# Kernel tuning notes

Measured on AMD Instinct MI355X. Metric: run time of the kernel, lower is better.

Reference implementation:

```python
import jax, jax.numpy as jnp
import numpy as np

N = 100000   # nodes
E = 600000   # edges
D = 128      # d_model
R = 200      # num_relations


def setup_inputs() -> dict:
    key = jax.random.key(0)
    ks = jax.random.split(key, 12)
    def nrm(k, shape, scale=0.02):
        return jax.random.normal(k, shape, jnp.float32) * scale
    return dict(
        node_features=jax.random.normal(ks[0], (N, D), jnp.float32),
        edge_index=jax.random.randint(ks[1], (2, E), 0, N),
        edge_type=jax.random.randint(ks[2], (E,), 0, R),
        rel_embed=nrm(ks[3], (R, D)),
        msg_w1=nrm(ks[4], (2 * D, D)), msg_b1=jnp.zeros((D,), jnp.float32),
        msg_w2=nrm(ks[5], (D, D)), msg_b2=jnp.zeros((D,), jnp.float32),
        attn_w1=nrm(ks[6], (2 * D, D)), attn_b1=jnp.zeros((D,), jnp.float32),
        attn_w2=nrm(ks[7], (D, 1)), attn_b2=jnp.zeros((1,), jnp.float32),
        ln1_g=jnp.ones((D,), jnp.float32), ln1_b=jnp.zeros((D,), jnp.float32),
        ffn_w1=nrm(ks[8], (D, 4 * D)), ffn_b1=jnp.zeros((4 * D,), jnp.float32),
        ffn_w2=nrm(ks[9], (4 * D, D)), ffn_b2=jnp.zeros((D,), jnp.float32),
        ln2_g=jnp.ones((D,), jnp.float32), ln2_b=jnp.zeros((D,), jnp.float32),
    )


def layer_norm(x, g, b, eps=1e-5):
    mu = x.mean(-1, keepdims=True)
    var = ((x - mu) ** 2).mean(-1, keepdims=True)
    return (x - mu) * jax.lax.rsqrt(var + eps) * g + b


def reference(node_features, edge_index, edge_type, rel_embed,
              msg_w1, msg_b1, msg_w2, msg_b2,
              attn_w1, attn_b1, attn_w2, attn_b2,
              ln1_g, ln1_b, ffn_w1, ffn_b1, ffn_w2, ffn_b2,
              ln2_g, ln2_b):
    Nn = node_features.shape[0]
    src, dst = edge_index[0], edge_index[1]
    # gather + edge message MLP
    src_feat = node_features[src]              # [E, D]
    rel_feat = rel_embed[edge_type]            # [E, D]
    h = jnp.concatenate([src_feat, rel_feat], axis=-1)          # [E, 2D]
    messages = jax.nn.relu(h @ msg_w1 + msg_b1) @ msg_w2 + msg_b2  # [E, D]
    # edge attention logits
    a_in = jnp.concatenate([node_features[dst], messages], axis=-1)  # [E, 2D]
    attn_raw = (jax.nn.leaky_relu(a_in @ attn_w1 + attn_b1, 0.2) @ attn_w2 + attn_b2)[:, 0]  # [E]
    # two-pass segment softmax over destination nodes
    attn_max = jax.ops.segment_max(attn_raw, dst, num_segments=Nn)   # [N]
    attn_exp = jnp.exp(attn_raw - attn_max[dst])                      # [E]
    attn_sum = jax.ops.segment_sum(attn_exp, dst, num_segments=Nn)   # [N]
    attn_w = attn_exp / (attn_sum[dst] + 1e-8)                        # [E]
    # scatter-add weighted messages
    aggr = jax.ops.segment_sum(attn_w[:, None] * messages, dst, num_segments=Nn)  # [N, D]
    x = layer_norm(node_features + aggr, ln1_g, ln1_b)
    ffn = jax.nn.gelu(x @ ffn_w1 + ffn_b1, approximate=False) @ ffn_w2 + ffn_b2
    return layer_norm(x + ffn, ln2_g, ln2_b)
```

## Files before the change

kernel.cpp:

```cpp
#include <hip/hip_runtime.h>
#include <hip/hip_bf16.h>

#define NN 100000
#define NE 600000
#define DD 128
#define RR 200
#define SCAN_NB ((NN + 255) / 256)

typedef __attribute__((ext_vector_type(8))) short bf16x8;
typedef __attribute__((ext_vector_type(4))) float f32x4;

__device__ __forceinline__ unsigned int bfbits(float x) {
    return (unsigned int)__builtin_bit_cast(unsigned short, __float2bfloat16(x));
}
__device__ __forceinline__ unsigned int pk2(float a, float b) {
    return bfbits(a) | (bfbits(b) << 16);
}
__device__ __forceinline__ unsigned short bf16s(float x) {
    return __builtin_bit_cast(unsigned short, __float2bfloat16(x));
}
__device__ __forceinline__ float unbf(unsigned short u) {
    return __builtin_bit_cast(float, ((unsigned int)u) << 16);
}
__device__ __forceinline__ float unlo(unsigned int u) {
    return __builtin_bit_cast(float, u << 16);
}
__device__ __forceinline__ float unhi(unsigned int u) {
    return __builtin_bit_cast(float, u & 0xffff0000u);
}

__device__ __forceinline__ void gload_lds16(const void* g, void* l) {
    __builtin_amdgcn_global_load_lds(
        (const __attribute__((address_space(1))) void*)g,
        (__attribute__((address_space(3))) void*)l, 16, 0, 0);
}

__global__ void k_initc(int* __restrict__ cnt) {
    int i = blockIdx.x * 256 + threadIdx.x;
    if (i < NN) cnt[i] = 0;
}

__global__ void k_hist(const int* __restrict__ dst, int* __restrict__ cnt) {
    int e = blockIdx.x * 256 + threadIdx.x;
    if (e < NE) atomicAdd(&cnt[dst[e]], 1);
}

__global__ void k_scanA(const int* __restrict__ cnt, int* __restrict__ bsum) {
    __shared__ int red[256];
    int i = blockIdx.x * 256 + threadIdx.x;
    red[threadIdx.x] = (i < NN) ? cnt[i] : 0;
    __syncthreads();
    for (int off = 128; off >= 1; off >>= 1) {
        if (threadIdx.x < off) red[threadIdx.x] += red[threadIdx.x + off];
        __syncthreads();
    }
    if (threadIdx.x == 0) bsum[blockIdx.x] = red[0];
}

__global__ void k_scanB(int* __restrict__ bsum) {
    __shared__ int sh[512];
    int t = threadIdx.x;
    int v = (t < SCAN_NB) ? bsum[t] : 0;
    sh[t] = v;
    __syncthreads();
    for (int off = 1; off < 512; off <<= 1) {
        int add = (t >= off) ? sh[t - off] : 0;
        __syncthreads();
        sh[t] += add;
        __syncthreads();
    }
    if (t < SCAN_NB) bsum[t] = sh[t] - v;
}

__global__ void k_scanC(const int* __restrict__ cnt, const int* __restrict__ bsum,
                        int* __restrict__ row_start, int* __restrict__ cursor) {
    __shared__ int sh[256];
    int i = blockIdx.x * 256 + threadIdx.x;
    int t = threadIdx.x;
    int v = (i < NN) ? cnt[i] : 0;
    sh[t] = v;
    __syncthreads();
    for (int off = 1; off < 256; off <<= 1) {
        int add = (t >= off) ? sh[t - off] : 0;
        __syncthreads();
        sh[t] += add;
        __syncthreads();
    }
    if (i < NN) {
        int ex = bsum[blockIdx.x] + sh[t] - v;
        row_start[i] = ex;
        cursor[i] = ex;
    }
}

__global__ void k_bucket(const int* __restrict__ src, const int* __restrict__ dst,
                         const int* __restrict__ etype, int* __restrict__ cursor,
                         int* __restrict__ srcs, int* __restrict__ ets,
                         int* __restrict__ dsts) {
    int e = blockIdx.x * 256 + threadIdx.x;
    if (e < NE) {
        int d = dst[e];
        int p = atomicAdd(&cursor[d], 1);
        srcs[p] = src[e];
        ets[p]  = etype[e];
        dsts[p] = d;
    }
}

__global__ void k_setup(const float* __restrict__ mw1, const float* __restrict__ mb1,
                        const float* __restrict__ mw2, const float* __restrict__ mb2,
                        const float* __restrict__ aw1, const float* __restrict__ rel,
                        const float* __restrict__ fw1, const float* __restrict__ fw2,
                        unsigned short* __restrict__ mw1p,
                        unsigned short* __restrict__ mw2p,
                        unsigned short* __restrict__ awTp,
                        unsigned short* __restrict__ mwBp,
                        unsigned short* __restrict__ fw1p,
                        unsigned short* __restrict__ fw2p,
                        unsigned short* __restrict__ relcb,
                        float* __restrict__ zb) {
    int idx = blockIdx.x * 256 + threadIdx.x;
    if (idx < 16384) {
        int i = idx & 7, l = (idx >> 3) & 63, ks = (idx >> 9) & 3, nt = idx >> 11;
        int k = ks * 32 + (l >> 4) * 8 + i, n = nt * 16 + (l & 15);
        mw1p[idx] = bf16s(mw1[k * 128 + n]);
    } else if (idx < 32768) {
        int j = idx - 16384;
        int i = j & 7, l = (j >> 3) & 63, ks = (j >> 9) & 3, nt = j >> 11;
        int k = ks * 32 + (l >> 4) * 8 + i, n = nt * 16 + (l & 15);
        mw2p[j] = bf16s(mw2[k * 128 + n]);
    } else if (idx < 49152) {
        int j = idx - 32768;
        int i = j & 7, l = (j >> 3) & 63, ks = (j >> 9) & 3, nt = j >> 11;
        int k = ks * 32 + (l >> 4) * 8 + i, n = nt * 16 + (l & 15);
        awTp[j] = bf16s(aw1[k * 128 + n]);
    } else if (idx < 65536) {
        int j = idx - 49152;
        int i = j & 7, l = (j >> 3) & 63, ks = (j >> 9) & 3, nt = j >> 11;
        int k = ks * 32 + (l >> 4) * 8 + i, n = nt * 16 + (l & 15);
        float s = 0.0f;
        for (int j2 = 0; j2 < 128; ++j2)
            s = fmaf(mw2[k * 128 + j2], aw1[(128 + j2) * 128 + n], s);
        mwBp[j] = bf16s(s);
    } else if (idx < 131072) {
        int j = idx - 65536;
        int i = j & 7, l = (j >> 3) & 63, ks = (j >> 9) & 3, nt = j >> 11;
        int k = ks * 32 + (l >> 4) * 8 + i, n = nt * 16 + (l & 15);
        fw1p[j] = bf16s(fw1[k * 512 + n]);
    } else if (idx < 196608) {
        int j = idx - 131072;
        int i = j & 7, l = (j >> 3) & 63, ks = (j >> 9) & 15, nt = j >> 13;
        int k = ks * 32 + (l >> 4) * 8 + i, n = nt * 16 + (l & 15);
        fw2p[j] = bf16s(fw2[k * 128 + n]);
    } else if (idx < 222208) {
        int j = idx - 196608;
        int r = j >> 7, n = j & 127;
        float s = mb1[n];
        for (int k = 0; k < 128; ++k)
            s = fmaf(rel[r * 128 + k], mw1[(128 + k) * 128 + n], s);
        relcb[j] = bf16s(s);
    } else if (idx < 222336) {
        int n = idx - 222208;
        float s = 0.0f;
        for (int j2 = 0; j2 < 128; ++j2)
            s = fmaf(mb2[j2], aw1[(128 + j2) * 128 + n], s);
        zb[n] = s;
    }
}

__global__ __launch_bounds__(256) void k_prepnfa(
    const float* __restrict__ nf, const unsigned short* __restrict__ awTp,
    const float* __restrict__ ab1,
    unsigned short* __restrict__ nfb, unsigned short* __restrict__ nfa)
{
    __shared__ alignas(16) unsigned short XB[64 * 128];
    const int t = threadIdx.x;
    const int w = t >> 6, l = t & 63;
    const int wm = w >> 1, wn = w & 1;
    const int lm = l & 15, lk = l >> 4;
    const int n0 = blockIdx.x * 64;

    {
        const int row = t >> 2, seg = t & 3;
        long ng = n0 + row; if (ng >= NN) ng = NN - 1;
        const float* sp = nf + ng * DD + seg * 32;
        uint4 o[4];
        #pragma unroll
        for (int i = 0; i < 4; ++i) {
            float4 f0 = *reinterpret_cast<const float4*>(sp + i * 8);
            float4 f1 = *reinterpret_cast<const float4*>(sp + i * 8 + 4);
            o[i].x = pk2(f0.x, f0.y); o[i].y = pk2(f0.z, f0.w);
            o[i].z = pk2(f1.x, f1.y); o[i].w = pk2(f1.z, f1.w);
        }
        if (n0 + row < NN) {
            #pragma unroll
            for (int i = 0; i < 4; ++i)
                *reinterpret_cast<uint4*>(&nfb[(size_t)(n0 + row) * DD + (seg * 4 + i) * 8]) = o[i];
        }
        #pragma unroll
        for (int i = 0; i < 4; ++i) {
            int c = seg * 4 + i, slot = c ^ (row & 7);
            *reinterpret_cast<uint4*>(&XB[row * 128 + slot * 8]) = o[i];
        }
    }
    __syncthreads();

    f32x4 acc[2][4];
    #pragma unroll
    for (int mf = 0; mf < 2; ++mf)
        #pragma unroll
        for (int nfr = 0; nfr < 4; ++nfr) acc[mf][nfr] = (f32x4){0.f, 0.f, 0.f, 0.f};

    #pragma unroll
    for (int ks = 0; ks < 4; ++ks) {
        bf16x8 a[2];
        #pragma unroll
        for (int mf = 0; mf < 2; ++mf) {
            int m = wm * 32 + mf * 16 + lm;
            int slot = (ks * 4 + lk) ^ (m & 7);
            a[mf] = *reinterpret_cast<const bf16x8*>(&XB[m * 128 + slot * 8]);
        }
        #pragma unroll
        for (int nfr = 0; nfr < 4; ++nfr) {
            int nt = wn * 4 + nfr;
            bf16x8 b = *reinterpret_cast<const bf16x8*>(&awTp[((nt * 4 + ks) * 64 + l) * 8]);
            acc[0][nfr] = __builtin_amdgcn_mfma_f32_16x16x32_bf16(a[0], b, acc[0][nfr], 0, 0, 0);
            acc[1][nfr] = __builtin_amdgcn_mfma_f32_16x16x32_bf16(a[1], b, acc[1][nfr], 0, 0, 0);
        }
    }
    __syncthreads();

    #pragma unroll
    for (int nfr = 0; nfr < 4; ++nfr) {
        int n = wn * 64 + nfr * 16 + lm;
        float bv = ab1[n];
        #pragma unroll
        for (int mf = 0; mf < 2; ++mf)
            #pragma unroll
            for (int r = 0; r < 4; ++r) {
                int m = wm * 32 + mf * 16 + lk * 4 + r;
                XB[m * 128 + n] = bf16s(acc[mf][nfr][r] + bv);
            }
    }
    __syncthreads();

    #pragma unroll
    for (int j = 0; j < 4; ++j) {
        int q = j * 256 + t;
        int row = q >> 4, c16 = q & 15;
        if (n0 + row < NN)
            *reinterpret_cast<uint4*>(&nfa[(size_t)(n0 + row) * DD + c16 * 8]) =
                *reinterpret_cast<const uint4*>(&XB[row * 128 + c16 * 8]);
    }
}

__global__ __launch_bounds__(512) void k_edge(
    const unsigned short* __restrict__ nfb, const int* __restrict__ srcs,
    const int* __restrict__ dsts, const int* __restrict__ ets,
    const unsigned short* __restrict__ nfa, const unsigned short* __restrict__ relcb,
    const unsigned short* __restrict__ mw1p, const unsigned short* __restrict__ mwBp,
    const float* __restrict__ zb, const float* __restrict__ aw2,
    const float* __restrict__ ab2,
    unsigned short* __restrict__ hid_out, float* __restrict__ attn_raw)
{
    __shared__ alignas(16) unsigned short S[64 * 128];
    __shared__ alignas(16) unsigned short H[64 * 128];
    __shared__ float RED[64][4];

    const int t = threadIdx.x;
    const int w = t >> 6, l = t & 63;
    const int wm = w >> 2, wn = w & 3;
    const int lm = l & 15, lk = l >> 4;
    const int lrow = l >> 4, lslot = l & 15;
    const int e0 = blockIdx.x * 64;

    #pragma unroll
    for (int it = 0; it < 2; ++it) {
        int rb = w * 8 + it * 4;
        int row = rb + lrow;
        int c = lslot ^ (row & 7);
        gload_lds16(nfb + (size_t)srcs[e0 + row] * DD + c * 8, &S[rb * 128]);
    }
    #pragma unroll
    for (int it = 0; it < 2; ++it) {
        int rb = w * 8 + it * 4;
        int row = rb + lrow;
        int c = lslot ^ (row & 7);
        gload_lds16(relcb + (size_t)ets[e0 + row] * DD + c * 8, &H[rb * 128]);
    }
    __syncthreads();

    {
        f32x4 acc1[2][2];
        #pragma unroll
        for (int mf = 0; mf < 2; ++mf)
            #pragma unroll
            for (int nfr = 0; nfr < 2; ++nfr) acc1[mf][nfr] = (f32x4){0.f, 0.f, 0.f, 0.f};

        #pragma unroll
        for (int ks = 0; ks < 4; ++ks) {
            bf16x8 a[2];
            #pragma unroll
            for (int mf = 0; mf < 2; ++mf) {
                int m = wm * 32 + mf * 16 + lm;
                int slot = (ks * 4 + lk) ^ (m & 7);
                a[mf] = *reinterpret_cast<const bf16x8*>(&S[m * 128 + slot * 8]);
            }
            #pragma unroll
            for (int nfr = 0; nfr < 2; ++nfr) {
                int nt = wn * 2 + nfr;
                bf16x8 b = *reinterpret_cast<const bf16x8*>(&mw1p[((nt * 4 + ks) * 64 + l) * 8]);
                acc1[0][nfr] = __builtin_amdgcn_mfma_f32_16x16x32_bf16(a[0], b, acc1[0][nfr], 0, 0, 0);
                acc1[1][nfr] = __builtin_amdgcn_mfma_f32_16x16x32_bf16(a[1], b, acc1[1][nfr], 0, 0, 0);
            }
        }
        #pragma unroll
        for (int nfr = 0; nfr < 2; ++nfr) {
            int n = (wn * 2 + nfr) * 16 + lm;
            #pragma unroll
            for (int mf = 0; mf < 2; ++mf)
                #pragma unroll
                for (int r = 0; r < 4; ++r) {
                    int m = wm * 32 + mf * 16 + lk * 4 + r;
                    int sl = m * 128 + ((n >> 3) ^ (m & 7)) * 8 + (n & 7);
                    float v = acc1[mf][nfr][r] + unbf(H[sl]);
                    v = fmaxf(v, 0.0f);
                    H[sl] = bf16s(v);
                }
        }
    }
    __syncthreads();

    #pragma unroll
    for (int j = 0; j < 2; ++j) {
        int q = j * 512 + t;
        int row = q >> 4, c16 = q & 15;
        int slot = c16 ^ (row & 7);
        *reinterpret_cast<uint4*>(&hid_out[(size_t)(e0 + row) * DD + c16 * 8]) =
            *reinterpret_cast<const uint4*>(&H[row * 128 + slot * 8]);
    }
    #pragma unroll
    for (int it = 0; it < 2; ++it) {
        int rb = w * 8 + it * 4;
        int row = rb + lrow;
        int c = lslot ^ (row & 7);
        gload_lds16(nfa + (size_t)dsts[e0 + row] * DD + c * 8, &S[rb * 128]);
    }

    f32x4 acc[2][2];
    #pragma unroll
    for (int mf = 0; mf < 2; ++mf)
        #pragma unroll
        for (int nfr = 0; nfr < 2; ++nfr) acc[mf][nfr] = (f32x4){0.f, 0.f, 0.f, 0.f};

    #pragma unroll
    for (int ks = 0; ks < 4; ++ks) {
        bf16x8 a[2];
        #pragma unroll
        for (int mf = 0; mf < 2; ++mf) {
            int m = wm * 32 + mf * 16 + lm;
            int slot = (ks * 4 + lk) ^ (m & 7);
            a[mf] = *reinterpret_cast<const bf16x8*>(&H[m * 128 + slot * 8]);
        }
        #pragma unroll
        for (int nfr = 0; nfr < 2; ++nfr) {
            int nt = wn * 2 + nfr;
            bf16x8 b = *reinterpret_cast<const bf16x8*>(&mwBp[((nt * 4 + ks) * 64 + l) * 8]);
            acc[0][nfr] = __builtin_amdgcn_mfma_f32_16x16x32_bf16(a[0], b, acc[0][nfr], 0, 0, 0);
            acc[1][nfr] = __builtin_amdgcn_mfma_f32_16x16x32_bf16(a[1], b, acc[1][nfr], 0, 0, 0);
        }
    }
    __syncthreads();

    {
        float zbv[2], aw2v[2];
        #pragma unroll
        for (int nfr = 0; nfr < 2; ++nfr) {
            int nc = (wn * 2 + nfr) * 16 + lm;
            zbv[nfr] = zb[nc];
            aw2v[nfr] = aw2[nc];
        }
        #pragma unroll
        for (int mf = 0; mf < 2; ++mf)
            #pragma unroll
            for (int r = 0; r < 4; ++r) {
                int m = wm * 32 + mf * 16 + lk * 4 + r;
                float s = 0.0f;
                #pragma unroll
                for (int nfr = 0; nfr < 2; ++nfr) {
                    int nc = (wn * 2 + nfr) * 16 + lm;
                    float v = acc[mf][nfr][r] + zbv[nfr]
                            + unbf(S[m * 128 + ((nc >> 3) ^ (m & 7)) * 8 + (nc & 7)]);
                    v = (v > 0.0f) ? v : 0.2f * v;
                    s = fmaf(v, aw2v[nfr], s);
                }
                s += __shfl_xor(s, 1, 64);
                s += __shfl_xor(s, 2, 64);
                s += __shfl_xor(s, 4, 64);
                s += __shfl_xor(s, 8, 64);
                if (lm == 0) RED[m][wn] = s;
            }
    }
    __syncthreads();

    if (t < 64) {
        attn_raw[e0 + t] = RED[t][0] + RED[t][1] + RED[t][2] + RED[t][3] + ab2[0];
    }
}

__global__ __launch_bounds__(256) void k_aggr(
    const unsigned short* __restrict__ hid, const float* __restrict__ raw,
    const int* __restrict__ row_start, const int* __restrict__ cnt,
    unsigned short* __restrict__ haggrb)
{
    const int l = threadIdx.x & 63;
    const int n = blockIdx.x * 4 + (threadIdx.x >> 6);
    if (n >= NN) return;
    const int rs = row_start[n], deg = cnt[n];

    float m = -INFINITY;
    for (int j = l; j < deg; j += 64) m = fmaxf(m, raw[rs + j]);
    #pragma unroll
    for (int off = 32; off >= 1; off >>= 1) m = fmaxf(m, __shfl_xor(m, off, 64));

    float s = 0.0f;
    for (int j = l; j < deg; j += 64) s += expf(raw[rs + j] - m);
    #pragma unroll
    for (int off = 32; off >= 1; off >>= 1) s += __shfl_xor(s, off, 64);
    const float rinv = 1.0f / (s + 1e-8f);

    float a0 = 0.0f, a1 = 0.0f;
    for (int j = 0; j < deg; ++j) {
        float w = expf(raw[rs + j] - m) * rinv;
        unsigned int v = *reinterpret_cast<const unsigned int*>(
            &hid[(size_t)(rs + j) * DD + l * 2]);
        a0 = fmaf(w, unlo(v), a0);
        a1 = fmaf(w, unhi(v), a1);
    }
    *reinterpret_cast<unsigned int*>(&haggrb[(size_t)n * DD + l * 2]) = pk2(a0, a1);
}

__global__ __launch_bounds__(512) void k_node(
    const float* __restrict__ nf, const unsigned short* __restrict__ haggrb,
    const unsigned short* __restrict__ mw2p, const float* __restrict__ mb2,
    const float* __restrict__ g1, const float* __restrict__ b1,
    const unsigned short* __restrict__ fw1p, const float* __restrict__ fb1,
    const unsigned short* __restrict__ fw2p, const float* __restrict__ fb2,
    const float* __restrict__ g2, const float* __restrict__ b2,
    float* __restrict__ out)
{
    __shared__ alignas(16) unsigned short XB[64 * 128];
    __shared__ alignas(16) unsigned short HB[64 * 256];

    const int t = threadIdx.x;
    const int w = t >> 6, l = t & 63;
    const int wm = w >> 2, wn = w & 3;
    const int lm = l & 15, lk = l >> 4;
    const int lrow = l >> 4, lslot = l & 15;
    const int row = t >> 3;
    const int q = t & 7;
    const long n0 = (long)blockIdx.x * 64;
    const long rg = n0 + row;
    const long rc = (rg < NN) ? rg : (NN - 1);

    unsigned short* HG = HB;
    #pragma unroll
    for (int it = 0; it < 2; ++it) {
        int rb = w * 8 + it * 4;
        int rr = rb + lrow;
        long grow = n0 + rr; if (grow >= NN) grow = NN - 1;
        int c = lslot ^ (rr & 7);
        gload_lds16(haggrb + grow * DD + c * 8, &HG[rb * 128]);
    }
    __syncthreads();

    {
        f32x4 acc0[2][2];
        #pragma unroll
        for (int mf = 0; mf < 2; ++mf)
            #pragma unroll
            for (int nfr = 0; nfr < 2; ++nfr) acc0[mf][nfr] = (f32x4){0.f, 0.f, 0.f, 0.f};

        #pragma unroll
        for (int ks = 0; ks < 4; ++ks) {
            bf16x8 a[2];
            #pragma unroll
            for (int mf = 0; mf < 2; ++mf) {
                int m = wm * 32 + mf * 16 + lm;
                int slot = (ks * 4 + lk) ^ (m & 7);
                a[mf] = *reinterpret_cast<const bf16x8*>(&HG[m * 128 + slot * 8]);
            }
            #pragma unroll
            for (int nfr = 0; nfr < 2; ++nfr) {
                int nt = wn * 2 + nfr;
                bf16x8 b = *reinterpret_cast<const bf16x8*>(&mw2p[((nt * 4 + ks) * 64 + l) * 8]);
                acc0[0][nfr] = __builtin_amdgcn_mfma_f32_16x16x32_bf16(a[0], b, acc0[0][nfr], 0, 0, 0);
                acc0[1][nfr] = __builtin_amdgcn_mfma_f32_16x16x32_bf16(a[1], b, acc0[1][nfr], 0, 0, 0);
            }
        }
        #pragma unroll
        for (int nfr = 0; nfr < 2; ++nfr) {
            int n = (wn * 2 + nfr) * 16 + lm;
            float bv = mb2[n];
            #pragma unroll
            for (int mf = 0; mf < 2; ++mf)
                #pragma unroll
                for (int r = 0; r < 4; ++r) {
                    int m = wm * 32 + mf * 16 + lk * 4 + r;
                    XB[m * 128 + ((n >> 3) ^ (m & 7)) * 8 + (n & 7)] = bf16s(acc0[mf][nfr][r] + bv);
                }
        }
    }
    __syncthreads();

    float xr[16];
    float s = 0.0f, ss = 0.0f;
    {
        const float* xp = nf + rc * DD + q * 16;
        #pragma unroll
        for (int i = 0; i < 2; ++i) {
            int c = q * 2 + i, slot = c ^ (row & 7);
            uint4 v = *reinterpret_cast<const uint4*>(&XB[row * 128 + slot * 8]);
            float f[8];
            f[0] = unlo(v.x); f[1] = unhi(v.x); f[2] = unlo(v.y); f[3] = unhi(v.y);
            f[4] = unlo(v.z); f[5] = unhi(v.z); f[6] = unlo(v.w); f[7] = unhi(v.w);
            float4 a = *reinterpret_cast<const float4*>(xp + i * 8);
            float4 b = *reinterpret_cast<const float4*>(xp + i * 8 + 4);
            float vv[8] = {a.x + f[0], a.y + f[1], a.z + f[2], a.w + f[3],
                           b.x + f[4], b.y + f[5], b.z + f[6], b.w + f[7]};
            #pragma unroll
            for (int j = 0; j < 8; ++j) {
                xr[i * 8 + j] = vv[j];
                s += vv[j];
                ss = fmaf(vv[j], vv[j], ss);
            }
        }
    }
    s  += __shfl_xor(s, 1, 64);  s  += __shfl_xor(s, 2, 64);  s  += __shfl_xor(s, 4, 64);
    ss += __shfl_xor(ss, 1, 64); ss += __shfl_xor(ss, 2, 64); ss += __shfl_xor(ss, 4, 64);
    {
        float mu = s * (1.0f / DD);
        float var = ss * (1.0f / DD) - mu * mu;
        float rstd = rsqrtf(var + 1e-5f);
        #pragma unroll
        for (int i = 0; i < 4; ++i) {
            float4 gv = *reinterpret_cast<const float4*>(g1 + q * 16 + i * 4);
            float4 bv = *reinterpret_cast<const float4*>(b1 + q * 16 + i * 4);
            xr[i * 4 + 0] = (xr[i * 4 + 0] - mu) * rstd * gv.x + bv.x;
            xr[i * 4 + 1] = (xr[i * 4 + 1] - mu) * rstd * gv.y + bv.y;
            xr[i * 4 + 2] = (xr[i * 4 + 2] - mu) * rstd * gv.z + bv.z;
            xr[i * 4 + 3] = (xr[i * 4 + 3] - mu) * rstd * gv.w + bv.w;
        }
        #pragma unroll
        for (int i = 0; i < 2; ++i) {
            int c = q * 2 + i, slot = c ^ (row & 7);
            uint4 v;
            v.x = pk2(xr[i * 8 + 0], xr[i * 8 + 1]);
            v.y = pk2(xr[i * 8 + 2], xr[i * 8 + 3]);
            v.z = pk2(xr[i * 8 + 4], xr[i * 8 + 5]);
            v.w = pk2(xr[i * 8 + 6], xr[i * 8 + 7]);
            *reinterpret_cast<uint4*>(&XB[row * 128 + slot * 8]) = v;
        }
    }
    __syncthreads();

    f32x4 acc2[2][2];
    #pragma unroll
    for (int mf = 0; mf < 2; ++mf)
        #pragma unroll
        for (int nfr = 0; nfr < 2; ++nfr) acc2[mf][nfr] = (f32x4){0.f, 0.f, 0.f, 0.f};

    #pragma unroll
    for (int half = 0; half < 2; ++half) {
        f32x4 acc[2][4];
        #pragma unroll
        for (int mf = 0; mf < 2; ++mf)
            #pragma unroll
            for (int nfr = 0; nfr < 4; ++nfr) acc[mf][nfr] = (f32x4){0.f, 0.f, 0.f, 0.f};

        #pragma unroll
        for (int ks = 0; ks < 4; ++ks) {
            bf16x8 a[2];
            #pragma unroll
            for (int mf = 0; mf < 2; ++mf) {
                int m = wm * 32 + mf * 16 + lm;
                int slot = (ks * 4 + lk) ^ (m & 7);
                a[mf] = *reinterpret_cast<const bf16x8*>(&XB[m * 128 + slot * 8]);
            }
            #pragma unroll
            for (int nfr = 0; nfr < 4; ++nfr) {
                int nt = half * 16 + wn * 4 + nfr;
                bf16x8 b = *reinterpret_cast<const bf16x8*>(&fw1p[((nt * 4 + ks) * 64 + l) * 8]);
                acc[0][nfr] = __builtin_amdgcn_mfma_f32_16x16x32_bf16(a[0], b, acc[0][nfr], 0, 0, 0);
                acc[1][nfr] = __builtin_amdgcn_mfma_f32_16x16x32_bf16(a[1], b, acc[1][nfr], 0, 0, 0);
            }
        }
        #pragma unroll
        for (int nfr = 0; nfr < 4; ++nfr) {
            int nl = (wn * 4 + nfr) * 16 + lm;
            float bv = fb1[half * 256 + nl];
            #pragma unroll
            for (int mf = 0; mf < 2; ++mf)
                #pragma unroll
                for (int r = 0; r < 4; ++r) {
                    int m = wm * 32 + mf * 16 + lk * 4 + r;
                    float h = acc[mf][nfr][r] + bv;
                    float e = __expf(h * -1.702f);
                    float gvv = h * __builtin_amdgcn_rcpf(1.0f + e);
                    HB[m * 256 + (((nl >> 3) ^ (m & 7)) * 8) + (nl & 7)] = bf16s(gvv);
                }
        }
        __syncthreads();

        #pragma unroll
        for (int ks = 0; ks < 8; ++ks) {
            bf16x8 a[2];
            #pragma unroll
            for (int mf = 0; mf < 2; ++mf) {
                int m = wm * 32 + mf * 16 + lm;
                int slot = (ks * 4 + lk) ^ (m & 7);
                a[mf] = *reinterpret_cast<const bf16x8*>(&HB[m * 256 + slot * 8]);
            }
            #pragma unroll
            for (int nfr = 0; nfr < 2; ++nfr) {
                int nt = wn * 2 + nfr;
                int kg = half * 8 + ks;
                bf16x8 b = *reinterpret_cast<const bf16x8*>(&fw2p[((nt * 16 + kg) * 64 + l) * 8]);
                acc2[0][nfr] = __builtin_amdgcn_mfma_f32_16x16x32_bf16(a[0], b, acc2[0][nfr], 0, 0, 0);
                acc2[1][nfr] = __builtin_amdgcn_mfma_f32_16x16x32_bf16(a[1], b, acc2[1][nfr], 0, 0, 0);
            }
        }
        __syncthreads();
    }

    #pragma unroll
    for (int nfr = 0; nfr < 2; ++nfr) {
        int n = (wn * 2 + nfr) * 16 + lm;
        float bv = fb2[n];
        #pragma unroll
        for (int mf = 0; mf < 2; ++mf)
            #pragma unroll
            for (int r = 0; r < 4; ++r) {
                int m = wm * 32 + mf * 16 + lk * 4 + r;
                XB[m * 128 + (((n >> 3) ^ (m & 7)) * 8) + (n & 7)] = bf16s(acc2[mf][nfr][r] + bv);
            }
    }
    __syncthreads();

    float s2 = 0.0f, ss2 = 0.0f;
    #pragma unroll
    for (int i = 0; i < 2; ++i) {
        int c = q * 2 + i, slot = c ^ (row & 7);
        uint4 v = *reinterpret_cast<const uint4*>(&XB[row * 128 + slot * 8]);
        float f[8];
        f[0] = unlo(v.x); f[1] = unhi(v.x); f[2] = unlo(v.y); f[3] = unhi(v.y);
        f[4] = unlo(v.z); f[5] = unhi(v.z); f[6] = unlo(v.w); f[7] = unhi(v.w);
        #pragma unroll
        for (int j = 0; j < 8; ++j) {
            float vv = xr[i * 8 + j] + f[j];
            xr[i * 8 + j] = vv;
            s2 += vv;
            ss2 = fmaf(vv, vv, ss2);
        }
    }
    s2  += __shfl_xor(s2, 1, 64);  s2  += __shfl_xor(s2, 2, 64);  s2  += __shfl_xor(s2, 4, 64);
    ss2 += __shfl_xor(ss2, 1, 64); ss2 += __shfl_xor(ss2, 2, 64); ss2 += __shfl_xor(ss2, 4, 64);
    {
        float mu = s2 * (1.0f / DD);
        float var = ss2 * (1.0f / DD) - mu * mu;
        float rstd = rsqrtf(var + 1e-5f);
        if (rg < NN) {
            float* op = out + rg * DD + q * 16;
            #pragma unroll
            for (int i = 0; i < 4; ++i) {
                float4 gv = *reinterpret_cast<const float4*>(g2 + q * 16 + i * 4);
                float4 bv = *reinterpret_cast<const float4*>(b2 + q * 16 + i * 4);
                float4 o;
                o.x = (xr[i * 4 + 0] - mu) * rstd * gv.x + bv.x;
                o.y = (xr[i * 4 + 1] - mu) * rstd * gv.y + bv.y;
                o.z = (xr[i * 4 + 2] - mu) * rstd * gv.z + bv.z;
                o.w = (xr[i * 4 + 3] - mu) * rstd * gv.w + bv.w;
                *reinterpret_cast<float4*>(op + i * 4) = o;
            }
        }
    }
}

extern "C" void kernel_launch(void* const* d_in, const int* in_sizes, int n_in,
                              void* d_out, int out_size, void* d_ws, size_t ws_size,
                              hipStream_t stream)
{
    const float* nf  = (const float*)d_in[0];
    const int*   ei  = (const int*)d_in[1];
    const int*   et  = (const int*)d_in[2];
    const float* rel = (const float*)d_in[3];
    const float* mw1 = (const float*)d_in[4];
    const float* mb1 = (const float*)d_in[5];
    const float* mw2 = (const float*)d_in[6];
    const float* mb2 = (const float*)d_in[7];
    const float* aw1 = (const float*)d_in[8];
    const float* ab1 = (const float*)d_in[9];
    const float* aw2 = (const float*)d_in[10];
    const float* ab2 = (const float*)d_in[11];
    const float* g1  = (const float*)d_in[12];
    const float* b1  = (const float*)d_in[13];
    const float* fw1 = (const float*)d_in[14];
    const float* fb1 = (const float*)d_in[15];
    const float* fw2 = (const float*)d_in[16];
    const float* fb2 = (const float*)d_in[17];
    const float* g2  = (const float*)d_in[18];
    const float* b2  = (const float*)d_in[19];
    float* out = (float*)d_out;

    char* ws = (char*)d_ws;
    size_t off = 0;
    auto alloc = [&](size_t bytes) -> char* {
        char* p = ws + off;
        off += (bytes + 255) & ~(size_t)255;
        return p;
    };
    unsigned short* hid = (unsigned short*)alloc((size_t)NE * DD * 2);
    float* attn_raw = (float*)alloc((size_t)NE * 4);
    unsigned short* haggrb = (unsigned short*)alloc((size_t)NN * DD * 2);
    unsigned short* nfa = (unsigned short*)alloc((size_t)NN * DD * 2);
    unsigned short* nfb = (unsigned short*)alloc((size_t)NN * DD * 2);
    unsigned short* relcb = (unsigned short*)alloc((size_t)RR * DD * 2);
    float* zb  = (float*)alloc((size_t)128 * 4);
    int* cnt       = (int*)alloc((size_t)NN * 4);
    int* row_start = (int*)alloc((size_t)NN * 4);
    int* cursor    = (int*)alloc((size_t)NN * 4);
    int* srcs      = (int*)alloc((size_t)NE * 4);
    int* ets       = (int*)alloc((size_t)NE * 4);
    int* dsts      = (int*)alloc((size_t)NE * 4);
    int* bsum      = (int*)alloc((size_t)SCAN_NB * 4);
    unsigned short* mw1p = (unsigned short*)alloc(16384 * 2);
    unsigned short* mw2p = (unsigned short*)alloc(16384 * 2);
    unsigned short* awTp = (unsigned short*)alloc(16384 * 2);
    unsigned short* mwBp = (unsigned short*)alloc(16384 * 2);
    unsigned short* fw1p = (unsigned short*)alloc(65536 * 2);
    unsigned short* fw2p = (unsigned short*)alloc(65536 * 2);

    const int* srcp = ei;
    const int* dstp = ei + NE;

    hipLaunchKernelGGL(k_initc, dim3(SCAN_NB), dim3(256), 0, stream, cnt);
    hipLaunchKernelGGL(k_hist, dim3((NE + 255) / 256), dim3(256), 0, stream, dstp, cnt);
    hipLaunchKernelGGL(k_scanA, dim3(SCAN_NB), dim3(256), 0, stream, cnt, bsum);
    hipLaunchKernelGGL(k_scanB, dim3(1), dim3(512), 0, stream, bsum);
    hipLaunchKernelGGL(k_scanC, dim3(SCAN_NB), dim3(256), 0, stream, cnt, bsum, row_start, cursor);
    hipLaunchKernelGGL(k_bucket, dim3((NE + 255) / 256), dim3(256), 0, stream,
                       srcp, dstp, et, cursor, srcs, ets, dsts);
    hipLaunchKernelGGL(k_setup, dim3(869), dim3(256), 0, stream,
                       mw1, mb1, mw2, mb2, aw1, rel, fw1, fw2,
                       mw1p, mw2p, awTp, mwBp, fw1p, fw2p, relcb, zb);
    hipLaunchKernelGGL(k_prepnfa, dim3((NN + 63) / 64), dim3(256), 0, stream,
                       nf, awTp, ab1, nfb, nfa);
    hipLaunchKernelGGL(k_edge, dim3(NE / 64), dim3(512), 0, stream,
                       nfb, srcs, dsts, ets, nfa, relcb,
                       mw1p, mwBp, zb, aw2, ab2,
                       hid, attn_raw);
    hipLaunchKernelGGL(k_aggr, dim3((NN + 3) / 4), dim3(256), 0, stream,
                       hid, attn_raw, row_start, cnt, haggrb);
    hipLaunchKernelGGL(k_node, dim3((NN + 63) / 64), dim3(512), 0, stream,
                       nf, haggrb, mw2p, mb2, g1, b1, fw1p, fb1, fw2p, fb2, g2, b2, out);
}
```

Baseline: 437.6 us.

## Fold count init into setup, cache softmax weights in LDS, shrink FFN chunking

Merges the count-zeroing kernel into the weight-setup kernel, removing one launch. In the aggregation kernel, each wave now computes 64 softmax weights in parallel into shared memory instead of every lane recomputing expf serially per edge. The node kernel processes the 512-wide FFN hidden layer in four 128-wide chunks instead of two 256-wide ones. This halves the HB shared buffer and the accumulator register count to raise occupancy, at the cost of more barriers and an extra sync.

```diff
diff --git a/kernel.cpp b/kernel.cpp
--- a/kernel.cpp
+++ b/kernel.cpp
@@ -33,11 +33,6 @@
     __builtin_amdgcn_global_load_lds(
         (const __attribute__((address_space(1))) void*)g,
         (__attribute__((address_space(3))) void*)l, 16, 0, 0);
-}
-
-__global__ void k_initc(int* __restrict__ cnt) {
-    int i = blockIdx.x * 256 + threadIdx.x;
-    if (i < NN) cnt[i] = 0;
 }
 
 __global__ void k_hist(const int* __restrict__ dst, int* __restrict__ cnt) {
@@ -118,7 +113,7 @@
                         unsigned short* __restrict__ fw1p,
                         unsigned short* __restrict__ fw2p,
                         unsigned short* __restrict__ relcb,
-                        float* __restrict__ zb) {
+                        float* __restrict__ zb, int* __restrict__ cnt) {
     int idx = blockIdx.x * 256 + threadIdx.x;
     if (idx < 16384) {
         int i = idx & 7, l = (idx >> 3) & 63, ks = (idx >> 9) & 3, nt = idx >> 11;
@@ -165,6 +160,8 @@
         for (int j2 = 0; j2 < 128; ++j2)
             s = fmaf(mb2[j2], aw1[(128 + j2) * 128 + n], s);
         zb[n] = s;
+    } else if (idx < 322336) {
+        cnt[idx - 222336] = 0;
     }
 }
 
@@ -413,8 +410,10 @@
     const int* __restrict__ row_start, const int* __restrict__ cnt,
     unsigned short* __restrict__ haggrb)
 {
+    __shared__ float wbuf[4][64];
     const int l = threadIdx.x & 63;
-    const int n = blockIdx.x * 4 + (threadIdx.x >> 6);
+    const int nib = threadIdx.x >> 6;
+    const int n = blockIdx.x * 4 + nib;
     if (n >= NN) return;
     const int rs = row_start[n], deg = cnt[n];
 
@@ -430,12 +429,16 @@
     const float rinv = 1.0f / (s + 1e-8f);
 
     float a0 = 0.0f, a1 = 0.0f;
-    for (int j = 0; j < deg; ++j) {
-        float w = expf(raw[rs + j] - m) * rinv;
-        unsigned int v = *reinterpret_cast<const unsigned int*>(
-            &hid[(size_t)(rs + j) * DD + l * 2]);
-        a0 = fmaf(w, unlo(v), a0);
-        a1 = fmaf(w, unhi(v), a1);
+    for (int base = 0; base < deg; base += 64) {
+        int ntc = min(64, deg - base);
+        if (l < ntc) wbuf[nib][l] = expf(raw[rs + base + l] - m) * rinv;
+        for (int j = 0; j < ntc; ++j) {
+            float w = wbuf[nib][j];
+            unsigned int v = *reinterpret_cast<const unsigned int*>(
+                &hid[(size_t)(rs + base + j) * DD + l * 2]);
+            a0 = fmaf(w, unlo(v), a0);
+            a1 = fmaf(w, unhi(v), a1);
+        }
     }
     *reinterpret_cast<unsigned int*>(&haggrb[(size_t)n * DD + l * 2]) = pk2(a0, a1);
 }
@@ -450,7 +453,7 @@
     float* __restrict__ out)
 {
     __shared__ alignas(16) unsigned short XB[64 * 128];
-    __shared__ alignas(16) unsigned short HB[64 * 256];
+    __shared__ alignas(16) unsigned short HB[64 * 128];
 
     const int t = threadIdx.x;
     const int w = t >> 6, l = t & 63;
@@ -498,6 +501,7 @@
                 acc0[1][nfr] = __builtin_amdgcn_mfma_f32_16x16x32_bf16(a[1], b, acc0[1][nfr], 0, 0, 0);
             }
         }
+        __syncthreads();
         #pragma unroll
         for (int nfr = 0; nfr < 2; ++nfr) {
             int n = (wn * 2 + nfr) * 16 + lm;
@@ -571,12 +575,12 @@
         for (int nfr = 0; nfr < 2; ++nfr) acc2[mf][nfr] = (f32x4){0.f, 0.f, 0.f, 0.f};
 
     #pragma unroll
-    for (int half = 0; half < 2; ++half) {
-        f32x4 acc[2][4];
+    for (int ch = 0; ch < 4; ++ch) {
+        f32x4 acc[2][2];
         #pragma unroll
         for (int mf = 0; mf < 2; ++mf)
             #pragma unroll
-            for (int nfr = 0; nfr < 4; ++nfr) acc[mf][nfr] = (f32x4){0.f, 0.f, 0.f, 0.f};
+            for (int nfr = 0; nfr < 2; ++nfr) acc[mf][nfr] = (f32x4){0.f, 0.f, 0.f, 0.f};
 
         #pragma unroll
         for (int ks = 0; ks < 4; ++ks) {
@@ -588,17 +592,17 @@
                 a[mf] = *reinterpret_cast<const bf16x8*>(&XB[m * 128 + slot * 8]);
             }
             #pragma unroll
-            for (int nfr = 0; nfr < 4; ++nfr) {
-                int nt = half * 16 + wn * 4 + nfr;
+            for (int nfr = 0; nfr < 2; ++nfr) {
+                int nt = ch * 8 + wn * 2 + nfr;
                 bf16x8 b = *reinterpret_cast<const bf16x8*>(&fw1p[((nt * 4 + ks) * 64 + l) * 8]);
                 acc[0][nfr] = __builtin_amdgcn_mfma_f32_16x16x32_bf16(a[0], b, acc[0][nfr], 0, 0, 0);
                 acc[1][nfr] = __builtin_amdgcn_mfma_f32_16x16x32_bf16(a[1], b, acc[1][nfr], 0, 0, 0);
             }
         }
         #pragma unroll
-        for (int nfr = 0; nfr < 4; ++nfr) {
-            int nl = (wn * 4 + nfr) * 16 + lm;
-            float bv = fb1[half * 256 + nl];
+        for (int nfr = 0; nfr < 2; ++nfr) {
+            int nl = (wn * 2 + nfr) * 16 + lm;
+            float bv = fb1[ch * 128 + nl];
             #pragma unroll
             for (int mf = 0; mf < 2; ++mf)
                 #pragma unroll
@@ -607,24 +611,24 @@
                     float h = acc[mf][nfr][r] + bv;
                     float e = __expf(h * -1.702f);
                     float gvv = h * __builtin_amdgcn_rcpf(1.0f + e);
-                    HB[m * 256 + (((nl >> 3) ^ (m & 7)) * 8) + (nl & 7)] = bf16s(gvv);
+                    HB[m * 128 + (((nl >> 3) ^ (m & 7)) * 8) + (nl & 7)] = bf16s(gvv);
                 }
         }
         __syncthreads();
 
         #pragma unroll
-        for (int ks = 0; ks < 8; ++ks) {
+        for (int ks = 0; ks < 4; ++ks) {
             bf16x8 a[2];
             #pragma unroll
             for (int mf = 0; mf < 2; ++mf) {
                 int m = wm * 32 + mf * 16 + lm;
                 int slot = (ks * 4 + lk) ^ (m & 7);
-                a[mf] = *reinterpret_cast<const bf16x8*>(&HB[m * 256 + slot * 8]);
+                a[mf] = *reinterpret_cast<const bf16x8*>(&HB[m * 128 + slot * 8]);
             }
             #pragma unroll
             for (int nfr = 0; nfr < 2; ++nfr) {
                 int nt = wn * 2 + nfr;
-                int kg = half * 8 + ks;
+                int kg = ch * 4 + ks;
                 bf16x8 b = *reinterpret_cast<const bf16x8*>(&fw2p[((nt * 16 + kg) * 64 + l) * 8]);
                 acc2[0][nfr] = __builtin_amdgcn_mfma_f32_16x16x32_bf16(a[0], b, acc2[0][nfr], 0, 0, 0);
                 acc2[1][nfr] = __builtin_amdgcn_mfma_f32_16x16x32_bf16(a[1], b, acc2[1][nfr], 0, 0, 0);
@@ -743,16 +747,15 @@
     const int* srcp = ei;
     const int* dstp = ei + NE;
 
-    hipLaunchKernelGGL(k_initc, dim3(SCAN_NB), dim3(256), 0, stream, cnt);
+    hipLaunchKernelGGL(k_setup, dim3(1260), dim3(256), 0, stream,
+                       mw1, mb1, mw2, mb2, aw1, rel, fw1, fw2,
+                       mw1p, mw2p, awTp, mwBp, fw1p, fw2p, relcb, zb, cnt);
     hipLaunchKernelGGL(k_hist, dim3((NE + 255) / 256), dim3(256), 0, stream, dstp, cnt);
     hipLaunchKernelGGL(k_scanA, dim3(SCAN_NB), dim3(256), 0, stream, cnt, bsum);
     hipLaunchKernelGGL(k_scanB, dim3(1), dim3(512), 0, stream, bsum);
     hipLaunchKernelGGL(k_scanC, dim3(SCAN_NB), dim3(256), 0, stream, cnt, bsum, row_start, cursor);
     hipLaunchKernelGGL(k_bucket, dim3((NE + 255) / 256), dim3(256), 0, stream,
                        srcp, dstp, et, cursor, srcs, ets, dsts);
-    hipLaunchKernelGGL(k_setup, dim3(869), dim3(256), 0, stream,
-                       mw1, mb1, mw2, mb2, aw1, rel, fw1, fw2,
-                       mw1p, mw2p, awTp, mwBp, fw1p, fw2p, relcb, zb);
     hipLaunchKernelGGL(k_prepnfa, dim3((NN + 63) / 64), dim3(256), 0, stream,
                        nf, awTp, ab1, nfb, nfa);
     hipLaunchKernelGGL(k_edge, dim3(NE / 64), dim3(512), 0, stream,
```

New measurement: 416.0 us. -4.9%, faster.
